# Kernel optimization log

Hardware: AMD Instinct MI355X
Metric: run time of the kernel (lower is better)

Reference implementation:

```python
import jax, jax.numpy as jnp
import numpy as np

B = 384
D_EMB = 256
NUM_TASKS = 4
MARGIN = 1.0
EPS = 1e-6  # F.pairwise_distance default eps, added to the difference


def setup_inputs() -> dict:
    key = jax.random.key(0)
    k1, k2 = jax.random.split(key)
    embeddings = jax.random.normal(k1, (B, D_EMB), dtype=jnp.float32)
    task_weights = jnp.ones((NUM_TASKS,), dtype=jnp.float32)
    task_rankings = jax.random.randint(k2, (B, NUM_TASKS), 0, 5, dtype=jnp.int32)
    return {"embeddings": embeddings, "task_weights": task_weights,
            "task_rankings": task_rankings}


def reference(embeddings, task_weights, task_rankings):
    # Pairwise euclidean distances, matching F.pairwise_distance: ||x - y + eps||_2
    diff = embeddings[:, None, :] - embeddings[None, :, :] + EPS      # [B, B, d]
    dist = jnp.sqrt(jnp.sum(diff * diff, axis=-1))                    # [B, B]

    # Triplet margin term for all (i, j, k): relu(D[i,j] - D[i,k] + margin)
    triple = jax.nn.relu(dist[:, :, None] - dist[:, None, :] + MARGIN)  # [B, B, B]

    total = jnp.zeros((), dtype=embeddings.dtype)
    for t in range(NUM_TASKS):  # small fixed loop over tasks
        r = task_rankings[:, t]
        gt = r[:, None] > r[None, :]                   # gt[a,b] = r[a] > r[b]
        mask = gt[:, :, None] & gt[None, :, :]         # (r_i>r_j) & (r_j>r_k)
        count = jnp.sum(mask).astype(embeddings.dtype)
        s = jnp.sum(jnp.where(mask, triple, jnp.zeros((), embeddings.dtype)))
        task_loss = s / jnp.maximum(count, 1.0)
        total = total + jnp.where(count > 0, task_weights[t] * task_loss, 0.0)
    return total
```

## Files before the change

### kernel.cpp

```cpp
#include <hip/hip_runtime.h>

#define NB   384
#define ND   256
#define EPSF 1e-6f
#define NBIN 512

#define WF_OFF   0
#define PART_OFF 16
#define ETP_OFF  1024

__device__ __forceinline__ unsigned bf16rne(float f) {
    const unsigned b = __float_as_uint(f);
    return (b + 0x7FFFu + ((b >> 16) & 1u)) >> 16;
}

__global__ __launch_bounds__(256) void prep_kernel(
    const float* __restrict__ emb,
    const float* __restrict__ tw,
    const int*   __restrict__ rank,
    float* __restrict__ ws)
{
    __shared__ float    t[32][33];
    __shared__ unsigned hist[20];

    const int tid = threadIdx.x;
    const int dt  = blockIdx.x & 7;
    const int jt  = blockIdx.x >> 3;
    const int c   = tid & 31;
    const int r8  = tid >> 5;

    #pragma unroll
    for (int p = 0; p < 4; ++p) {
        const int j = jt * 32 + r8 + p * 8;
        const int d = dt * 32 + c;
        t[r8 + p * 8][c] = emb[(size_t)j * ND + d];
    }
    __syncthreads();

    const int jloc = tid & 31;
    const int gl   = tid >> 5;
    const float v0 = t[jloc][gl * 4 + 0];
    const float v1 = t[jloc][gl * 4 + 1];
    const float v2 = t[jloc][gl * 4 + 2];
    const float v3 = t[jloc][gl * 4 + 3];
    uint2 o;
    o.x = bf16rne(v0) | (bf16rne(v1) << 16);
    o.y = bf16rne(v2) | (bf16rne(v3) << 16);
    uint2* etp = reinterpret_cast<uint2*>(ws + ETP_OFF);
    etp[(size_t)(dt * 8 + gl) * NB + jt * 32 + jloc] = o;

    if (blockIdx.x == 0) {
        if (tid < 20) hist[tid] = 0u;
        __syncthreads();
        for (int e = tid; e < NB * 4; e += 256)
            atomicAdd(&hist[(e & 3) * 5 + rank[e]], 1u);
        __syncthreads();
        if (tid < 4) {
            double cnt = 0.0;
            unsigned below = 0;
            #pragma unroll
            for (int v = 0; v < 5; ++v) {
                unsigned hv = hist[tid * 5 + v];
                unsigned above = (unsigned)NB - below - hv;
                cnt += (double)hv * (double)below * (double)above;
                below += hv;
            }
            ws[WF_OFF + tid] = (cnt > 0.0) ? (float)((double)tw[tid] / cnt) : 0.f;
        }
    }
}

__global__ __launch_bounds__(512) void loss_kernel(
    const float* __restrict__ emb,
    const uint2* __restrict__ etp,
    const int*   __restrict__ rank,
    const float* __restrict__ wf,
    float* __restrict__ partial)
{
    __shared__ unsigned hist[NBIN];
    __shared__ unsigned offs[NBIN + 1];
    __shared__ unsigned curs[NBIN];
    __shared__ unsigned srk[512];
    __shared__ unsigned long long cm[8][16];
    __shared__ unsigned cumtab[9][16];
    __shared__ unsigned wtot[8];
    __shared__ float    mmx[16];
    __shared__ float    sprm[2];
    __shared__ float    wfl[4];
    __shared__ float    red[8];

    const int p  = threadIdx.x;
    const int bi = blockIdx.x;
    const int wv = p >> 6;

    if (p < 4) wfl[p] = wf[p];
    hist[p] = 0u;
    if (p >= NB) srk[p] = 0xFFFFFFFFu;
    __syncthreads();

    float d = 0.f;
    if (p < NB) {
        const float* ei = emb + (size_t)bi * ND;
        float acc = 0.f;
        for (int g0 = 0; g0 < 64; g0 += 8) {
            uint2 l[8];
            #pragma unroll
            for (int u = 0; u < 8; ++u)
                l[u] = etp[(size_t)(g0 + u) * NB + p];
            #pragma unroll
            for (int u = 0; u < 8; ++u) {
                const int dd = (g0 + u) * 4;
                const float j0 = __uint_as_float(l[u].x << 16);
                const float j1 = __uint_as_float(l[u].x & 0xFFFF0000u);
                const float j2 = __uint_as_float(l[u].y << 16);
                const float j3 = __uint_as_float(l[u].y & 0xFFFF0000u);
                const float t0 = ei[dd + 0] - j0;
                const float t1 = ei[dd + 1] - j1;
                const float t2 = ei[dd + 2] - j2;
                const float t3 = ei[dd + 3] - j3;
                acc = fmaf(t0, t0, acc);
                acc = fmaf(t1, t1, acc);
                acc = fmaf(t2, t2, acc);
                acc = fmaf(t3, t3, acc);
            }
        }
        d = sqrtf(acc);
    }

    float dl = (p < NB) ? d : 3.0e38f;
    float dh = (p < NB) ? d : -3.0e38f;
    #pragma unroll
    for (int off = 32; off > 0; off >>= 1) {
        dl = fminf(dl, __shfl_xor(dl, off, 64));
        dh = fmaxf(dh, __shfl_xor(dh, off, 64));
    }
    if ((p & 63) == 0) { mmx[wv] = dl; mmx[8 + wv] = dh; }
    __syncthreads();
    if (p == 0) {
        float mn = mmx[0], mx = mmx[8];
        #pragma unroll
        for (int w = 1; w < 8; ++w) {
            mn = fminf(mn, mmx[w]);
            mx = fmaxf(mx, mmx[8 + w]);
        }
        int S = (int)(511.0f / (mx - mn + 1.0f));
        if (S < 1) S = 1;
        sprm[0] = mn;
        sprm[1] = (float)S;
    }
    __syncthreads();
    const float dmin   = sprm[0];
    const float scaleF = sprm[1];
    const int   S      = (int)scaleF;

    int q = 0;
    unsigned rpk = 0xFFFFFFFFu;
    if (p < NB) {
        q = (int)((d - dmin) * scaleF);
        if (q > NBIN - 1) q = NBIN - 1;
        atomicAdd(&hist[q], 1u);
        const int4 r4 = *reinterpret_cast<const int4*>(rank + p * 4);
        rpk = (unsigned)r4.x | ((unsigned)r4.y << 8) |
              ((unsigned)r4.z << 16) | ((unsigned)r4.w << 24);
    }
    __syncthreads();

    const unsigned h = hist[p];
    unsigned inc = h;
    #pragma unroll
    for (int s = 1; s < 64; s <<= 1) {
        const unsigned o = __shfl_up(inc, s, 64);
        if ((p & 63) >= s) inc += o;
    }
    if ((p & 63) == 63) wtot[wv] = inc;
    __syncthreads();
    unsigned woff = 0;
    for (int w = 0; w < wv; ++w) woff += wtot[w];
    const unsigned excl = woff + inc - h;
    offs[p] = excl;
    curs[p] = excl;
    if (p == NBIN - 1) offs[NBIN] = excl + h;
    __syncthreads();

    if (p < NB) {
        const unsigned pos = atomicAdd(&curs[q], 1u);
        srk[pos] = rpk;
    }
    __syncthreads();

    const unsigned rsv = srk[p];
    #pragma unroll
    for (int t = 0; t < 4; ++t) {
        const unsigned rt = (rsv >> (8 * t)) & 0xFFu;
        #pragma unroll
        for (int w = 0; w < 4; ++w) {
            const unsigned long long m = __ballot(rt <= (unsigned)w);
            if ((p & 63) == 0) cm[wv][t * 4 + w] = m;
        }
    }
    __syncthreads();
    if (p < 16) {
        unsigned c = 0;
        #pragma unroll
        for (int w2 = 0; w2 < 8; ++w2) {
            cumtab[w2][p] = c;
            c += (unsigned)__popcll(cm[w2][p]);
        }
        cumtab[8][p] = c;
    }
    __syncthreads();

    float contrib = 0.f;
    if (p < NB) {
        const float thr = d + 1.0f;
        const int jidx = (q + S > NBIN) ? NBIN : (q + S);
        const int kidx = (q - S + 1 < 0) ? 0 : (q - S + 1);
        const unsigned P = offs[jidx];
        const unsigned L = offs[kidx];
        const int Pwv = (int)(P >> 6), Lwv = (int)(L >> 6);
        const unsigned long long Pmask = (1ull << (P & 63)) - 1ull;
        const unsigned long long Lmask = (1ull << (L & 63)) - 1ull;

        const int4 ri4 = *reinterpret_cast<const int4*>(rank + bi * 4);
        const unsigned rip = (unsigned)ri4.x | ((unsigned)ri4.y << 8) |
                             ((unsigned)ri4.z << 16) | ((unsigned)ri4.w << 24);

        float jacc = 0.f, kacc = 0.f;
        #pragma unroll
        for (int t = 0; t < 4; ++t) {
            const int ri = (int)((rip >> (8 * t)) & 0xFFu);
            const int ro = (int)((rpk >> (8 * t)) & 0xFFu);
            const float wt = wfl[t];
            if (ro > 0 && ro < ri) {
                const int w = t * 4 + (ro - 1);
                const unsigned N = cumtab[Pwv][w] +
                                   (unsigned)__popcll(cm[Pwv][w] & Pmask);
                jacc += wt * (float)N;
            }
            if (ro + 1 < ri) {
                const int wh = t * 4 + (ri - 1);
                const int wl = t * 4 + ro;
                const unsigned cLh = cumtab[Lwv][wh] +
                                     (unsigned)__popcll(cm[Lwv][wh] & Lmask);
                const unsigned cLl = cumtab[Lwv][wl] +
                                     (unsigned)__popcll(cm[Lwv][wl] & Lmask);
                const unsigned C = (cumtab[8][wh] - cLh) - (cumtab[8][wl] - cLl);
                kacc += wt * (float)C;
            }
        }
        contrib = jacc * thr - kacc * d;
    }

    #pragma unroll
    for (int off = 32; off > 0; off >>= 1)
        contrib += __shfl_down(contrib, off);
    if ((p & 63) == 0) red[wv] = contrib;
    __syncthreads();
    if (p == 0) {
        float s = 0.f;
        #pragma unroll
        for (int w = 0; w < 8; ++w) s += red[w];
        partial[bi] = s;
    }
}

__global__ __launch_bounds__(256) void reduce_kernel(
    const float* __restrict__ partial, float* __restrict__ out)
{
    __shared__ float r[4];
    const int tid = threadIdx.x;
    float t = 0.f;
    for (int p = tid; p < NB; p += 256) t += partial[p];
    #pragma unroll
    for (int off = 32; off > 0; off >>= 1)
        t += __shfl_down(t, off);
    if ((tid & 63) == 0) r[tid >> 6] = t;
    __syncthreads();
    if (tid == 0) out[0] = r[0] + r[1] + r[2] + r[3];
}

extern "C" void kernel_launch(void* const* d_in, const int* in_sizes, int n_in,
                              void* d_out, int out_size, void* d_ws, size_t ws_size,
                              hipStream_t stream)
{
    (void)in_sizes; (void)n_in; (void)out_size; (void)ws_size;
    const float* emb  = (const float*)d_in[0];
    const float* tw   = (const float*)d_in[1];
    const int*   rank = (const int*)d_in[2];
    float* ws  = (float*)d_ws;
    float* out = (float*)d_out;

    prep_kernel<<<96, 256, 0, stream>>>(emb, tw, rank, ws);
    loss_kernel<<<NB, 512, 0, stream>>>(
        emb, reinterpret_cast<const uint2*>(ws + ETP_OFF), rank,
        ws + WF_OFF, ws + PART_OFF);
    reduce_kernel<<<1, 256, 0, stream>>>(ws + PART_OFF, out);
}
```

Baseline: 23.42 us.

## Fuse final reduction into loss kernel via last-block ticket and shrink block to NB

Drops the separate reduce kernel. Each loss block publishes its partial sum with a release store and takes a ticket from an atomic counter, and the last block to arrive sums all partials and writes the output. The loss block size also shrinks from 512 to 384 threads so no lanes sit idle, and the histogram bin count drops to match. EPS is folded into the bf16-converted embedding copy, and the self-distance is excluded from the min used for binning. This removes one kernel launch but adds atomics and fences, and changes quantisation granularity and the eps handling.

```diff
diff --git a/kernel.cpp b/kernel.cpp
--- a/kernel.cpp
+++ b/kernel.cpp
@@ -3,9 +3,10 @@
 #define NB   384
 #define ND   256
 #define EPSF 1e-6f
-#define NBIN 512
+#define NBIN 384
 
 #define WF_OFF   0
+#define TICK_OFF 8
 #define PART_OFF 16
 #define ETP_OFF  1024
 
@@ -39,10 +40,10 @@
 
     const int jloc = tid & 31;
     const int gl   = tid >> 5;
-    const float v0 = t[jloc][gl * 4 + 0];
-    const float v1 = t[jloc][gl * 4 + 1];
-    const float v2 = t[jloc][gl * 4 + 2];
-    const float v3 = t[jloc][gl * 4 + 3];
+    const float v0 = t[jloc][gl * 4 + 0] - EPSF;
+    const float v1 = t[jloc][gl * 4 + 1] - EPSF;
+    const float v2 = t[jloc][gl * 4 + 2] - EPSF;
+    const float v3 = t[jloc][gl * 4 + 3] - EPSF;
     uint2 o;
     o.x = bf16rne(v0) | (bf16rne(v1) << 16);
     o.y = bf16rne(v2) | (bf16rne(v3) << 16);
@@ -50,6 +51,8 @@
     etp[(size_t)(dt * 8 + gl) * NB + jt * 32 + jloc] = o;
 
     if (blockIdx.x == 0) {
+        if (tid == 0)
+            *reinterpret_cast<unsigned*>(ws + TICK_OFF) = 0u;
         if (tid < 20) hist[tid] = 0u;
         __syncthreads();
         for (int e = tid; e < NB * 4; e += 256)
@@ -70,80 +73,79 @@
     }
 }
 
-__global__ __launch_bounds__(512) void loss_kernel(
+__global__ __launch_bounds__(NB) void loss_kernel(
     const float* __restrict__ emb,
     const uint2* __restrict__ etp,
     const int*   __restrict__ rank,
     const float* __restrict__ wf,
-    float* __restrict__ partial)
+    float*       __restrict__ partial,
+    unsigned*    __restrict__ tick,
+    float*       __restrict__ out)
 {
     __shared__ unsigned hist[NBIN];
     __shared__ unsigned offs[NBIN + 1];
     __shared__ unsigned curs[NBIN];
-    __shared__ unsigned srk[512];
-    __shared__ unsigned long long cm[8][16];
-    __shared__ unsigned cumtab[9][16];
-    __shared__ unsigned wtot[8];
-    __shared__ float    mmx[16];
+    __shared__ unsigned srk[NB];
+    __shared__ unsigned long long cm[7][17];
+    __shared__ unsigned cumtab[7][17];
+    __shared__ unsigned wtot[6];
+    __shared__ float    mmx[12];
     __shared__ float    sprm[2];
     __shared__ float    wfl[4];
-    __shared__ float    red[8];
+    __shared__ float    red[6];
+    __shared__ int      lastflag;
 
     const int p  = threadIdx.x;
     const int bi = blockIdx.x;
     const int wv = p >> 6;
 
-    if (p < 4) wfl[p] = wf[p];
+    if (p < 4)  wfl[p] = wf[p];
+    if (p < 17) cm[6][p] = 0ull;
     hist[p] = 0u;
-    if (p >= NB) srk[p] = 0xFFFFFFFFu;
-    __syncthreads();
-
-    float d = 0.f;
-    if (p < NB) {
-        const float* ei = emb + (size_t)bi * ND;
-        float acc = 0.f;
-        for (int g0 = 0; g0 < 64; g0 += 8) {
-            uint2 l[8];
-            #pragma unroll
-            for (int u = 0; u < 8; ++u)
-                l[u] = etp[(size_t)(g0 + u) * NB + p];
-            #pragma unroll
-            for (int u = 0; u < 8; ++u) {
-                const int dd = (g0 + u) * 4;
-                const float j0 = __uint_as_float(l[u].x << 16);
-                const float j1 = __uint_as_float(l[u].x & 0xFFFF0000u);
-                const float j2 = __uint_as_float(l[u].y << 16);
-                const float j3 = __uint_as_float(l[u].y & 0xFFFF0000u);
-                const float t0 = ei[dd + 0] - j0;
-                const float t1 = ei[dd + 1] - j1;
-                const float t2 = ei[dd + 2] - j2;
-                const float t3 = ei[dd + 3] - j3;
-                acc = fmaf(t0, t0, acc);
-                acc = fmaf(t1, t1, acc);
-                acc = fmaf(t2, t2, acc);
-                acc = fmaf(t3, t3, acc);
-            }
-        }
-        d = sqrtf(acc);
-    }
-
-    float dl = (p < NB) ? d : 3.0e38f;
-    float dh = (p < NB) ? d : -3.0e38f;
+
+    const float* ei = emb + (size_t)bi * ND;
+    float acc = 0.f;
+    for (int g0 = 0; g0 < 64; g0 += 8) {
+        uint2 l[8];
+        #pragma unroll
+        for (int u = 0; u < 8; ++u)
+            l[u] = etp[(size_t)(g0 + u) * NB + p];
+        #pragma unroll
+        for (int u = 0; u < 8; ++u) {
+            const int dd = (g0 + u) * 4;
+            const float j0 = __uint_as_float(l[u].x << 16);
+            const float j1 = __uint_as_float(l[u].x & 0xFFFF0000u);
+            const float j2 = __uint_as_float(l[u].y << 16);
+            const float j3 = __uint_as_float(l[u].y & 0xFFFF0000u);
+            const float t0 = ei[dd + 0] - j0;
+            const float t1 = ei[dd + 1] - j1;
+            const float t2 = ei[dd + 2] - j2;
+            const float t3 = ei[dd + 3] - j3;
+            acc = fmaf(t0, t0, acc);
+            acc = fmaf(t1, t1, acc);
+            acc = fmaf(t2, t2, acc);
+            acc = fmaf(t3, t3, acc);
+        }
+    }
+    const float d = sqrtf(acc);
+
+    float dl = (p == bi) ? 3.0e38f : d;
+    float dh = d;
     #pragma unroll
     for (int off = 32; off > 0; off >>= 1) {
         dl = fminf(dl, __shfl_xor(dl, off, 64));
         dh = fmaxf(dh, __shfl_xor(dh, off, 64));
     }
-    if ((p & 63) == 0) { mmx[wv] = dl; mmx[8 + wv] = dh; }
+    if ((p & 63) == 0) { mmx[wv] = dl; mmx[6 + wv] = dh; }
     __syncthreads();
     if (p == 0) {
-        float mn = mmx[0], mx = mmx[8];
-        #pragma unroll
-        for (int w = 1; w < 8; ++w) {
+        float mn = mmx[0], mx = mmx[6];
+        #pragma unroll
+        for (int w = 1; w < 6; ++w) {
             mn = fminf(mn, mmx[w]);
-            mx = fmaxf(mx, mmx[8 + w]);
-        }
-        int S = (int)(511.0f / (mx - mn + 1.0f));
+            mx = fmaxf(mx, mmx[6 + w]);
+        }
+        int S = (int)(383.0f / (mx - mn + 1.0f));
         if (S < 1) S = 1;
         sprm[0] = mn;
         sprm[1] = (float)S;
@@ -153,16 +155,13 @@
     const float scaleF = sprm[1];
     const int   S      = (int)scaleF;
 
-    int q = 0;
-    unsigned rpk = 0xFFFFFFFFu;
-    if (p < NB) {
-        q = (int)((d - dmin) * scaleF);
-        if (q > NBIN - 1) q = NBIN - 1;
-        atomicAdd(&hist[q], 1u);
-        const int4 r4 = *reinterpret_cast<const int4*>(rank + p * 4);
-        rpk = (unsigned)r4.x | ((unsigned)r4.y << 8) |
-              ((unsigned)r4.z << 16) | ((unsigned)r4.w << 24);
-    }
+    int q = (int)((d - dmin) * scaleF);
+    if (q < 0) q = 0;
+    if (q > NBIN - 1) q = NBIN - 1;
+    atomicAdd(&hist[q], 1u);
+    const int4 r4 = *reinterpret_cast<const int4*>(rank + p * 4);
+    const unsigned rpk = (unsigned)r4.x | ((unsigned)r4.y << 8) |
+                         ((unsigned)r4.z << 16) | ((unsigned)r4.w << 24);
     __syncthreads();
 
     const unsigned h = hist[p];
@@ -182,10 +181,8 @@
     if (p == NBIN - 1) offs[NBIN] = excl + h;
     __syncthreads();
 
-    if (p < NB) {
-        const unsigned pos = atomicAdd(&curs[q], 1u);
-        srk[pos] = rpk;
-    }
+    const unsigned pos = atomicAdd(&curs[q], 1u);
+    srk[pos] = rpk;
     __syncthreads();
 
     const unsigned rsv = srk[p];
@@ -202,54 +199,51 @@
     if (p < 16) {
         unsigned c = 0;
         #pragma unroll
-        for (int w2 = 0; w2 < 8; ++w2) {
+        for (int w2 = 0; w2 < 6; ++w2) {
             cumtab[w2][p] = c;
             c += (unsigned)__popcll(cm[w2][p]);
         }
-        cumtab[8][p] = c;
-    }
-    __syncthreads();
-
-    float contrib = 0.f;
-    if (p < NB) {
-        const float thr = d + 1.0f;
-        const int jidx = (q + S > NBIN) ? NBIN : (q + S);
-        const int kidx = (q - S + 1 < 0) ? 0 : (q - S + 1);
-        const unsigned P = offs[jidx];
-        const unsigned L = offs[kidx];
-        const int Pwv = (int)(P >> 6), Lwv = (int)(L >> 6);
-        const unsigned long long Pmask = (1ull << (P & 63)) - 1ull;
-        const unsigned long long Lmask = (1ull << (L & 63)) - 1ull;
-
-        const int4 ri4 = *reinterpret_cast<const int4*>(rank + bi * 4);
-        const unsigned rip = (unsigned)ri4.x | ((unsigned)ri4.y << 8) |
-                             ((unsigned)ri4.z << 16) | ((unsigned)ri4.w << 24);
-
-        float jacc = 0.f, kacc = 0.f;
-        #pragma unroll
-        for (int t = 0; t < 4; ++t) {
-            const int ri = (int)((rip >> (8 * t)) & 0xFFu);
-            const int ro = (int)((rpk >> (8 * t)) & 0xFFu);
-            const float wt = wfl[t];
-            if (ro > 0 && ro < ri) {
-                const int w = t * 4 + (ro - 1);
-                const unsigned N = cumtab[Pwv][w] +
-                                   (unsigned)__popcll(cm[Pwv][w] & Pmask);
-                jacc += wt * (float)N;
-            }
-            if (ro + 1 < ri) {
-                const int wh = t * 4 + (ri - 1);
-                const int wl = t * 4 + ro;
-                const unsigned cLh = cumtab[Lwv][wh] +
-                                     (unsigned)__popcll(cm[Lwv][wh] & Lmask);
-                const unsigned cLl = cumtab[Lwv][wl] +
-                                     (unsigned)__popcll(cm[Lwv][wl] & Lmask);
-                const unsigned C = (cumtab[8][wh] - cLh) - (cumtab[8][wl] - cLl);
-                kacc += wt * (float)C;
-            }
-        }
-        contrib = jacc * thr - kacc * d;
-    }
+        cumtab[6][p] = c;
+    }
+    __syncthreads();
+
+    const float thr = d + 1.0f;
+    const int jidx = (q + S > NBIN) ? NBIN : (q + S);
+    const int kidx = (q - S + 1 < 0) ? 0 : (q - S + 1);
+    const unsigned P = offs[jidx];
+    const unsigned L = offs[kidx];
+    const int Pwv = (int)(P >> 6), Lwv = (int)(L >> 6);
+    const unsigned long long Pmask = (1ull << (P & 63)) - 1ull;
+    const unsigned long long Lmask = (1ull << (L & 63)) - 1ull;
+
+    const int4 ri4 = *reinterpret_cast<const int4*>(rank + bi * 4);
+    const unsigned rip = (unsigned)ri4.x | ((unsigned)ri4.y << 8) |
+                         ((unsigned)ri4.z << 16) | ((unsigned)ri4.w << 24);
+
+    float jacc = 0.f, kacc = 0.f;
+    #pragma unroll
+    for (int t = 0; t < 4; ++t) {
+        const int ri = (int)((rip >> (8 * t)) & 0xFFu);
+        const int ro = (int)((rpk >> (8 * t)) & 0xFFu);
+        const float wt = wfl[t];
+        if (ro > 0 && ro < ri) {
+            const int w = t * 4 + (ro - 1);
+            const unsigned N = cumtab[Pwv][w] +
+                               (unsigned)__popcll(cm[Pwv][w] & Pmask);
+            jacc += wt * (float)N;
+        }
+        if (ro + 1 < ri) {
+            const int wh = t * 4 + (ri - 1);
+            const int wl = t * 4 + ro;
+            const unsigned cLh = cumtab[Lwv][wh] +
+                                 (unsigned)__popcll(cm[Lwv][wh] & Lmask);
+            const unsigned cLl = cumtab[Lwv][wl] +
+                                 (unsigned)__popcll(cm[Lwv][wl] & Lmask);
+            const unsigned C = (cumtab[6][wh] - cLh) - (cumtab[6][wl] - cLl);
+            kacc += wt * (float)C;
+        }
+    }
+    float contrib = jacc * thr - kacc * d;
 
     #pragma unroll
     for (int off = 32; off > 0; off >>= 1)
@@ -259,24 +253,31 @@
     if (p == 0) {
         float s = 0.f;
         #pragma unroll
-        for (int w = 0; w < 8; ++w) s += red[w];
-        partial[bi] = s;
-    }
-}
-
-__global__ __launch_bounds__(256) void reduce_kernel(
-    const float* __restrict__ partial, float* __restrict__ out)
-{
-    __shared__ float r[4];
-    const int tid = threadIdx.x;
-    float t = 0.f;
-    for (int p = tid; p < NB; p += 256) t += partial[p];
-    #pragma unroll
-    for (int off = 32; off > 0; off >>= 1)
-        t += __shfl_down(t, off);
-    if ((tid & 63) == 0) r[tid >> 6] = t;
-    __syncthreads();
-    if (tid == 0) out[0] = r[0] + r[1] + r[2] + r[3];
+        for (int w = 0; w < 6; ++w) s += red[w];
+        __hip_atomic_store(&partial[bi], s, __ATOMIC_RELEASE,
+                           __HIP_MEMORY_SCOPE_AGENT);
+        const unsigned t = __hip_atomic_fetch_add(tick, 1u, __ATOMIC_ACQ_REL,
+                                                  __HIP_MEMORY_SCOPE_AGENT);
+        lastflag = (t == NB - 1) ? 1 : 0;
+    }
+    __syncthreads();
+
+    if (lastflag) {
+        __threadfence();
+        float v = __hip_atomic_load(&partial[p], __ATOMIC_RELAXED,
+                                    __HIP_MEMORY_SCOPE_AGENT);
+        #pragma unroll
+        for (int off = 32; off > 0; off >>= 1)
+            v += __shfl_down(v, off);
+        if ((p & 63) == 0) red[wv] = v;
+        __syncthreads();
+        if (p == 0) {
+            float s = 0.f;
+            #pragma unroll
+            for (int w = 0; w < 6; ++w) s += red[w];
+            out[0] = s;
+        }
+    }
 }
 
 extern "C" void kernel_launch(void* const* d_in, const int* in_sizes, int n_in,
@@ -291,8 +292,8 @@
     float* out = (float*)d_out;
 
     prep_kernel<<<96, 256, 0, stream>>>(emb, tw, rank, ws);
-    loss_kernel<<<NB, 512, 0, stream>>>(
+    loss_kernel<<<NB, NB, 0, stream>>>(
         emb, reinterpret_cast<const uint2*>(ws + ETP_OFF), rank,
-        ws + WF_OFF, ws + PART_OFF);
-    reduce_kernel<<<1, 256, 0, stream>>>(ws + PART_OFF, out);
-}
+        ws + WF_OFF, ws + PART_OFF,
+        reinterpret_cast<unsigned*>(ws + TICK_OFF), out);
+}
```

Result: slower. 28.51 us (+21.7%).
